# Kernel tuning notes

Measured on AMD Instinct MI355X. Metric: run time of the kernel, lower is better.

The kernel has to match this reference:

```python
import jax, jax.numpy as jnp
import numpy as np

BS, NQ, NCLS = 16, 128, 3
T, P = 480, 72          # total targets, points per curve
COST_CLASS_W = 1.0
CURVES_W = 1.0
LOWER_W = 1.0
UPPER_W = 1.0


def setup_inputs() -> dict:
    key = jax.random.key(0)
    k1, k2, k3, k4, k5, k6, k7 = jax.random.split(key, 7)
    pred_logits = jax.random.normal(k1, (BS, NQ, NCLS), dtype=jnp.float32)
    pred_curves = jax.random.uniform(k2, (BS, NQ, 8), dtype=jnp.float32)
    # targets: [T, 5 + 2P] = [class_id, lower_y, upper_y, lower_x, upper_x, xs(P), ys(P)]
    ids = jax.random.randint(k3, (T,), 0, NCLS).astype(jnp.float32)
    ends = jax.random.uniform(k4, (T, 4), dtype=jnp.float32)  # ly, uy, lx, ux
    xs = jax.random.uniform(k5, (T, P), dtype=jnp.float32)
    ys = jax.random.uniform(k6, (T, P), dtype=jnp.float32)
    # variable number of valid points per lane; invalid points marked x = -1
    counts = jax.random.randint(k7, (T,), P // 2, P + 1)
    valid = jnp.arange(P)[None, :] < counts[:, None]
    xs = jnp.where(valid, xs, -1.0)
    targets = jnp.concatenate([ids[:, None], ends, xs, ys], axis=1)
    return {"pred_logits": pred_logits, "pred_curves": pred_curves, "targets": targets}


def reference(pred_logits, pred_curves, targets):
    bs, nq, _ = pred_logits.shape
    BN = bs * nq
    out_prob = jax.nn.softmax(pred_logits.reshape(BN, -1), axis=-1)
    tgt_ids = targets[:, 0].astype(jnp.int32)
    cost_class = -out_prob[:, tgt_ids]                      # [BN, T]

    ob = pred_curves.reshape(BN, 8)
    ly, uy, lx, ux = targets[:, 1], targets[:, 2], targets[:, 3], targets[:, 4]
    # L1 cdist on scalars == abs diff; averaged over (y, x) endpoint coords
    cost_lower = 0.5 * (jnp.abs(ob[:, 0:1] - ly[None, :]) + jnp.abs(ob[:, 2:3] - lx[None, :]))
    cost_upper = 0.5 * (jnp.abs(ob[:, 1:2] - uy[None, :]) + jnp.abs(ob[:, 3:4] - ux[None, :]))

    p = (targets.shape[1] - 5) // 2
    txs = targets[:, 5:5 + p]                               # [T, P]
    tys = targets[:, 5 + p:]                                # [T, P]
    valid = txs >= 0                                        # [T, P]
    per = jnp.sum(valid, axis=1).astype(jnp.float32)        # [T]
    total = jnp.sum(valid).astype(jnp.float32)
    w = jnp.sqrt(total / per)
    w = w / jnp.max(w)                                      # [T]

    p1 = jnp.stack([lx, ly], axis=-1)                       # [T, 2]
    p2 = jnp.stack([ux, uy], axis=-1)
    d = p2 - p1                                             # [T, 2]
    pi = jnp.stack([txs, tys], axis=-1)                     # [T, P, 2]
    p1pi = pi - p1[:, None, :]
    dot = jnp.einsum('tk,tpk->tp', d, p1pi)                 # [T, P]
    nrm = jnp.sqrt(jnp.sum(d * d, axis=-1))                 # [T]
    # original: proj = dot / nrm, then lam = proj / nrm
    lam = (dot / nrm[:, None]) / nrm[:, None]               # [T, P]

    a3, a2 = ob[:, 4], ob[:, 5]
    a1 = ob[:, 3] - a3 - a2 - ob[:, 2]
    a0 = ob[:, 2]
    b3, b2 = ob[:, 6], ob[:, 7]
    b1 = ob[:, 1] - b3 - b2 - ob[:, 0]
    b0 = ob[:, 0]

    L = lam[:, :, None]                                     # [T, P, 1] broadcast vs [BN]
    L2 = L * L
    L3 = L2 * L
    ox = a3 * L3 + a2 * L2 + a1 * L + a0                    # [T, P, BN]
    oy = b3 * L3 + b2 * L2 + b1 * L + b0

    diff = (txs[:, :, None] - ox) ** 2 + (tys[:, :, None] - oy) ** 2
    cost_polys = jnp.sum(jnp.where(valid[:, :, None], diff, 0.0), axis=1)  # [T, BN]
    cost_polys = cost_polys.T * w[None, :]                  # [BN, T]

    C = (COST_CLASS_W * cost_class + CURVES_W * cost_polys / 10.0
         + LOWER_W * cost_lower + UPPER_W * cost_upper)
    return C.reshape(bs, nq, -1)
```

## Files before the change

### kernel.cpp

```cpp
#include <hip/hip_runtime.h>
#include <math.h>

#define BS   16
#define NQ   128
#define NCLS 3
#define T    480
#define P    72
#define BN   (BS * NQ)
#define TROW (5 + 2 * P)
#define BNB  4

#define MD_OFF_B 0
#define EF_OFF_B 61440

__global__ __launch_bounds__(64) void moments_kernel(const float* __restrict__ targets,
                                                     double* __restrict__ MD,
                                                     float* __restrict__ EF) {
    int t    = blockIdx.x;
    int lane = threadIdx.x;
    const float* row = targets + (size_t)t * TROW;
    float ly = row[1], uy = row[2], lx = row[3], ux = row[4];
    float dx = ux - lx, dy = uy - ly;
    float nrm = sqrtf(dx * dx + dy * dy);

    double v[17];
#pragma unroll
    for (int i = 0; i < 17; ++i) v[i] = 0.0;

    for (int p = lane; p < P; p += 64) {
        float tx = row[5 + p];
        float ty = row[5 + P + p];
        if (tx >= 0.0f) {
            float lamf = dx * (tx - lx) + dy * (ty - ly);
            lamf = lamf / nrm / nrm;
            double L   = (double)lamf;
            double txd = (double)tx, tyd = (double)ty;
            double lp = 1.0;
#pragma unroll
            for (int j = 0; j < 7; ++j) {
                v[j] += lp;
                if (j < 4) {
                    v[7 + j]  += txd * lp;
                    v[11 + j] += tyd * lp;
                }
                lp *= L;
            }
            v[15] += txd * txd + tyd * tyd;
            v[16] += 1.0;
        }
    }

#pragma unroll
    for (int off = 32; off > 0; off >>= 1) {
#pragma unroll
        for (int i = 0; i < 17; ++i) v[i] += __shfl_down(v[i], off);
    }

    if (lane == 0) {
#pragma unroll
        for (int j = 0; j < 7; ++j) MD[j * T + t] = v[j];
#pragma unroll
        for (int k = 0; k < 4; ++k) {
            MD[(7 + k) * T + t]  = -2.0 * v[7 + k];
            MD[(11 + k) * T + t] = -2.0 * v[11 + k];
        }
        MD[15 * T + t] = v[15];
        EF[0 * T + t] = ly;
        EF[1 * T + t] = uy;
        EF[2 * T + t] = lx;
        EF[3 * T + t] = ux;
        EF[4 * T + t] = (float)v[16];
        EF[5 * T + t] = row[0];
    }
}

__global__ __launch_bounds__(512) void cost_kernel(const float* __restrict__ logits,
                                                   const float* __restrict__ curves,
                                                   const double* __restrict__ MD,
                                                   const float* __restrict__ EF,
                                                   float* __restrict__ out) {
    __shared__ float wavemin[8];
    int t    = threadIdx.x;
    int bn0  = blockIdx.x * BNB;
    int lane = t & 63;
    int wid  = t >> 6;

    float per = (t < T) ? EF[4 * T + t] : 1e30f;
    float pm = per;
#pragma unroll
    for (int off = 32; off > 0; off >>= 1) pm = fminf(pm, __shfl_xor(pm, off));
    if (lane == 0) wavemin[wid] = pm;
    __syncthreads();
    float per_min = wavemin[0];
#pragma unroll
    for (int i = 1; i < 8; ++i) per_min = fminf(per_min, wavemin[i]);

    if (t >= T) return;
    float w = sqrtf(per_min / per);

    double m[16];
#pragma unroll
    for (int r = 0; r < 16; ++r) m[r] = MD[r * T + t];
    float ly = EF[0 * T + t], uy = EF[1 * T + t];
    float lx = EF[2 * T + t], ux = EF[3 * T + t];
    int   id = (int)EF[5 * T + t];

#pragma unroll
    for (int j = 0; j < BNB; ++j) {
        int bn = bn0 + j;
        const float* ob = curves + (size_t)bn * 8;
        float o0 = ob[0], o1 = ob[1], o2 = ob[2], o3 = ob[3];
        float o4 = ob[4], o5 = ob[5], o6 = ob[6], o7 = ob[7];
        float a0 = o2, a1 = o3 - o4 - o5 - o2, a2 = o5, a3 = o4;
        float b0 = o0, b1 = o1 - o6 - o7 - o0, b2 = o7, b3 = o6;

        double A0 = a0, A1 = a1, A2 = a2, A3 = a3;
        double B0 = b0, B1 = b1, B2 = b2, B3 = b3;
        double acc = m[15]
            + (A0 * A0 + B0 * B0) * m[0]
            + 2.0 * (A0 * A1 + B0 * B1) * m[1]
            + (2.0 * (A0 * A2 + B0 * B2) + A1 * A1 + B1 * B1) * m[2]
            + 2.0 * (A0 * A3 + A1 * A2 + B0 * B3 + B1 * B2) * m[3]
            + (2.0 * (A1 * A3 + B1 * B3) + A2 * A2 + B2 * B2) * m[4]
            + 2.0 * (A2 * A3 + B2 * B3) * m[5]
            + (A3 * A3 + B3 * B3) * m[6]
            + A0 * m[7]  + A1 * m[8]  + A2 * m[9]  + A3 * m[10]
            + B0 * m[11] + B1 * m[12] + B2 * m[13] + B3 * m[14];

        const float* lg = logits + (size_t)bn * NCLS;
        float l0 = lg[0], l1 = lg[1], l2 = lg[2];
        float mx = fmaxf(l0, fmaxf(l1, l2));
        float e0 = __expf(l0 - mx), e1 = __expf(l1 - mx), e2 = __expf(l2 - mx);
        float inv = 1.0f / (e0 + e1 + e2);
        float prob = (id == 0) ? e0 * inv : ((id == 1) ? e1 * inv : e2 * inv);

        float cp = (float)acc * w * 0.1f;
        float cl = 0.5f * (fabsf(b0 - ly) + fabsf(a0 - lx));
        float cu = 0.5f * (fabsf(o1 - uy) + fabsf(o3 - ux));
        out[(size_t)bn * T + t] = -prob + cp + cl + cu;
    }
}

extern "C" void kernel_launch(void* const* d_in, const int* in_sizes, int n_in,
                              void* d_out, int out_size, void* d_ws, size_t ws_size,
                              hipStream_t stream) {
    const float* logits  = (const float*)d_in[0];
    const float* curves  = (const float*)d_in[1];
    const float* targets = (const float*)d_in[2];
    float* out = (float*)d_out;
    char*  ws  = (char*)d_ws;

    double* MD = (double*)(ws + MD_OFF_B);
    float*  EF = (float*) (ws + EF_OFF_B);

    moments_kernel<<<T, 64, 0, stream>>>(targets, MD, EF);
    cost_kernel<<<BN / BNB, 512, 0, stream>>>(logits, curves, MD, EF, out);
}
```

Baseline: 66.74 us.

## Fuse moment precomputation into cost kernel using shared memory per block

New measurement: 125.0 us. 1.87x slower.

```diff
diff --git a/kernel.cpp b/kernel.cpp
--- a/kernel.cpp
+++ b/kernel.cpp
@@ -8,106 +8,97 @@
 #define P    72
 #define BN   (BS * NQ)
 #define TROW (5 + 2 * P)
-#define BNB  4
+#define KBN  8
+#define NTHR 1024
 
-#define MD_OFF_B 0
-#define EF_OFF_B 61440
+__global__ __launch_bounds__(NTHR) void fused_kernel(
+    const float* __restrict__ logits,
+    const float* __restrict__ curves,
+    const float* __restrict__ targets,
+    float* __restrict__ out)
+{
+    __shared__ double sMD[16 * T];
+    __shared__ float  sPER[T];
+    __shared__ float  swm[16];
 
-__global__ __launch_bounds__(64) void moments_kernel(const float* __restrict__ targets,
-                                                     double* __restrict__ MD,
-                                                     float* __restrict__ EF) {
-    int t    = blockIdx.x;
-    int lane = threadIdx.x;
-    const float* row = targets + (size_t)t * TROW;
-    float ly = row[1], uy = row[2], lx = row[3], ux = row[4];
-    float dx = ux - lx, dy = uy - ly;
-    float nrm = sqrtf(dx * dx + dy * dy);
+    const int tid = threadIdx.x;
 
-    double v[17];
+    if (tid < 2 * T) {
+        const int t    = tid >> 1;
+        const int half = tid & 1;
+        const float* row = targets + (size_t)t * TROW;
+        const float ly = row[1], uy = row[2], lx = row[3], ux = row[4];
+        const float dx = ux - lx, dy = uy - ly;
+        const float nrm = sqrtf(dx * dx + dy * dy);
+
+        double v[17];
 #pragma unroll
-    for (int i = 0; i < 17; ++i) v[i] = 0.0;
+        for (int i = 0; i < 17; ++i) v[i] = 0.0;
 
-    for (int p = lane; p < P; p += 64) {
-        float tx = row[5 + p];
-        float ty = row[5 + P + p];
-        if (tx >= 0.0f) {
-            float lamf = dx * (tx - lx) + dy * (ty - ly);
-            lamf = lamf / nrm / nrm;
-            double L   = (double)lamf;
-            double txd = (double)tx, tyd = (double)ty;
-            double lp = 1.0;
+        const int p0 = half * (P / 2);
+        for (int p = p0; p < p0 + P / 2; ++p) {
+            float tx = row[5 + p];
+            float ty = row[5 + P + p];
+            if (tx >= 0.0f) {
+                float lamf = dx * (tx - lx) + dy * (ty - ly);
+                lamf = lamf / nrm / nrm;
+                double L   = (double)lamf;
+                double txd = (double)tx, tyd = (double)ty;
+                double lp  = 1.0;
 #pragma unroll
-            for (int j = 0; j < 7; ++j) {
-                v[j] += lp;
-                if (j < 4) {
-                    v[7 + j]  += txd * lp;
-                    v[11 + j] += tyd * lp;
+                for (int j = 0; j < 7; ++j) {
+                    v[j] += lp;
+                    if (j < 4) { v[7 + j] += txd * lp; v[11 + j] += tyd * lp; }
+                    lp *= L;
                 }
-                lp *= L;
+                v[15] += txd * txd + tyd * tyd;
+                v[16] += 1.0;
             }
-            v[15] += txd * txd + tyd * tyd;
-            v[16] += 1.0;
+        }
+#pragma unroll
+        for (int i = 0; i < 17; ++i) v[i] += __shfl_down(v[i], 1);
+
+        if (half == 0) {
+#pragma unroll
+            for (int j = 0; j < 7; ++j) sMD[j * T + t] = v[j];
+#pragma unroll
+            for (int k = 0; k < 4; ++k) {
+                sMD[(7 + k)  * T + t] = -2.0 * v[7 + k];
+                sMD[(11 + k) * T + t] = -2.0 * v[11 + k];
+            }
+            sMD[15 * T + t] = v[15];
+            sPER[t] = (float)v[16];
         }
     }
+    __syncthreads();
 
-#pragma unroll
-    for (int off = 32; off > 0; off >>= 1) {
-#pragma unroll
-        for (int i = 0; i < 17; ++i) v[i] += __shfl_down(v[i], off);
-    }
-
-    if (lane == 0) {
-#pragma unroll
-        for (int j = 0; j < 7; ++j) MD[j * T + t] = v[j];
-#pragma unroll
-        for (int k = 0; k < 4; ++k) {
-            MD[(7 + k) * T + t]  = -2.0 * v[7 + k];
-            MD[(11 + k) * T + t] = -2.0 * v[11 + k];
-        }
-        MD[15 * T + t] = v[15];
-        EF[0 * T + t] = ly;
-        EF[1 * T + t] = uy;
-        EF[2 * T + t] = lx;
-        EF[3 * T + t] = ux;
-        EF[4 * T + t] = (float)v[16];
-        EF[5 * T + t] = row[0];
-    }
-}
-
-__global__ __launch_bounds__(512) void cost_kernel(const float* __restrict__ logits,
-                                                   const float* __restrict__ curves,
-                                                   const double* __restrict__ MD,
-                                                   const float* __restrict__ EF,
-                                                   float* __restrict__ out) {
-    __shared__ float wavemin[8];
-    int t    = threadIdx.x;
-    int bn0  = blockIdx.x * BNB;
-    int lane = t & 63;
-    int wid  = t >> 6;
-
-    float per = (t < T) ? EF[4 * T + t] : 1e30f;
-    float pm = per;
+    float pm = (tid < T) ? sPER[tid] : 1e30f;
 #pragma unroll
     for (int off = 32; off > 0; off >>= 1) pm = fminf(pm, __shfl_xor(pm, off));
-    if (lane == 0) wavemin[wid] = pm;
+    if ((tid & 63) == 0) swm[tid >> 6] = pm;
     __syncthreads();
-    float per_min = wavemin[0];
+    float per_min = swm[0];
 #pragma unroll
-    for (int i = 1; i < 8; ++i) per_min = fminf(per_min, wavemin[i]);
+    for (int i = 1; i < 16; ++i) per_min = fminf(per_min, swm[i]);
 
+    const int g = tid >> 9;
+    const int t = tid & 511;
     if (t >= T) return;
-    float w = sqrtf(per_min / per);
 
     double m[16];
 #pragma unroll
-    for (int r = 0; r < 16; ++r) m[r] = MD[r * T + t];
-    float ly = EF[0 * T + t], uy = EF[1 * T + t];
-    float lx = EF[2 * T + t], ux = EF[3 * T + t];
-    int   id = (int)EF[5 * T + t];
+    for (int r = 0; r < 16; ++r) m[r] = sMD[r * T + t];
 
+    const float* row = targets + (size_t)t * TROW;
+    const float ly = row[1], uy = row[2], lx = row[3], ux = row[4];
+    const int   id = (int)row[0];
+    const float per = sPER[t];
+    const float w = sqrtf(per_min / per);
+
+    const int bnbase = blockIdx.x * KBN + g * (KBN / 2);
 #pragma unroll
-    for (int j = 0; j < BNB; ++j) {
-        int bn = bn0 + j;
+    for (int j = 0; j < KBN / 2; ++j) {
+        const int bn = bnbase + j;
         const float* ob = curves + (size_t)bn * 8;
         float o0 = ob[0], o1 = ob[1], o2 = ob[2], o3 = ob[3];
         float o4 = ob[4], o5 = ob[5], o6 = ob[6], o7 = ob[7];
@@ -147,12 +138,8 @@
     const float* logits  = (const float*)d_in[0];
     const float* curves  = (const float*)d_in[1];
     const float* targets = (const float*)d_in[2];
-    float* out = (float*)d_out;
-    char*  ws  = (char*)d_ws;
+    (void)d_ws; (void)ws_size;
 
-    double* MD = (double*)(ws + MD_OFF_B);
-    float*  EF = (float*) (ws + EF_OFF_B);
-
-    moments_kernel<<<T, 64, 0, stream>>>(targets, MD, EF);
-    cost_kernel<<<BN / BNB, 512, 0, stream>>>(logits, curves, MD, EF, out);
+    fused_kernel<<<BN / KBN, NTHR, 0, stream>>>(logits, curves, targets,
+                                                (float*)d_out);
 }
```
